# Kernel tuning notes

Hardware: AMD Instinct MI355X
Metric: run time of the kernel (lower is better)

The kernel has to match this reference:

```python
import jax, jax.numpy as jnp
import numpy as np

B, T, H, S, NH = 8, 4096, 1024, 64, 16
DH = H // NH
L = T // S  # tokens per sentence (contiguous partition)


def setup_inputs() -> dict:
    key = jax.random.key(0)
    ks = jax.random.split(key, 10)
    init = lambda k, shape: (jax.random.normal(k, shape, dtype=jnp.float32) * 0.02)
    starts = jnp.arange(S, dtype=jnp.int32) * L
    bounds = jnp.stack([starts, starts + L], axis=-1)  # [S,2]
    sentence_boundaries = jnp.broadcast_to(bounds, (B, S, 2))
    return {
        "context_hidden": jax.random.normal(ks[0], (B, T, H), dtype=jnp.float32),
        "sentence_boundaries": sentence_boundaries,
        "in_proj_w": init(ks[1], (3 * H, H)),
        "in_proj_b": jnp.zeros((3 * H,), jnp.float32),
        "out_w": init(ks[2], (H, H)),
        "out_b": jnp.zeros((H,), jnp.float32),
        "w1": init(ks[3], (H, 2 * H)),
        "b1": jnp.zeros((H,), jnp.float32),
        "w2": init(ks[4], (1, H)),
        "b2": jnp.zeros((1,), jnp.float32),
    }


def _forward(h, sentence_boundaries, in_proj_w, in_proj_b, out_w, out_b, w1, b1, w2, b2):
    starts = sentence_boundaries[:, :, 0]  # [B,S]
    ends = sentence_boundaries[:, :, 1]    # [B,S]
    t = jnp.arange(T, dtype=jnp.int32)
    # membership: token t belongs to sentence s iff start <= t < end
    member = (t[None, :, None] >= starts[:, None, :]) & (t[None, :, None] < ends[:, None, :])  # [B,T,S]
    mf = member.astype(h.dtype)
    counts = jnp.clip(mf.sum(axis=1), 1.0)  # [B,S]
    # segment mean pooling (encode_sentences)
    sent_repr = jnp.einsum('bts,bth->bsh', mf, h) / counts[..., None]  # [B,S,H]

    # multihead self-attention over sentence reprs (eval mode, no dropout)
    qkv = sent_repr @ in_proj_w.T + in_proj_b  # [B,S,3H]
    q, k, v = jnp.split(qkv, 3, axis=-1)
    q = q.reshape(B, S, NH, DH)
    k = k.reshape(B, S, NH, DH)
    v = v.reshape(B, S, NH, DH)
    scores = jnp.einsum('bqhd,bkhd->bhqk', q, k) / jnp.sqrt(jnp.asarray(DH, h.dtype))
    attn = jax.nn.softmax(scores, axis=-1)
    ctx = jnp.einsum('bhqk,bkhd->bqhd', attn, v).reshape(B, S, H)
    attended = ctx @ out_w.T + out_b  # [B,S,H]

    # gather each token's sentence repr
    sid = jnp.clip(member.astype(jnp.int32).argmax(axis=-1), 0, S - 1)  # [B,T]
    covered = member.any(axis=-1)  # [B,T]
    att_tok = jnp.take_along_axis(attended, sid[..., None], axis=1)  # [B,T,H]

    # coherence scorer MLP on concat([token, sent_repr]) without materializing concat
    hid = jax.nn.relu(h @ w1[:, :H].T + att_tok @ w1[:, H:].T + b1)  # [B,T,H]
    score = (hid @ w2.T + b2)[..., 0]  # [B,T]
    score = jnp.where(covered, score, 0.0)
    return h + score[..., None] * h


def reference(context_hidden, sentence_boundaries, in_proj_w, in_proj_b, out_w, out_b, w1, b1, w2, b2):
    return _forward(context_hidden, sentence_boundaries, in_proj_w, in_proj_b,
                    out_w, out_b, w1, b1, w2, b2)
```

## Files before the change

kernel.cpp:

```cpp
#include <hip/hip_runtime.h>
#include <stdint.h>

#define BB 8
#define TT 4096
#define HH 1024
#define SS 64
#define NHH 16
#define DHH 64

typedef __attribute__((ext_vector_type(8))) short short8;
typedef __attribute__((ext_vector_type(8))) unsigned short ushortx8;
typedef __attribute__((ext_vector_type(4))) float f32x4;
typedef unsigned short u16;

#define GLOAD16(gp, lp)                                                   \
  __builtin_amdgcn_global_load_lds(                                      \
      (const __attribute__((address_space(1))) void*)(gp),               \
      (__attribute__((address_space(3))) void*)(lp), 16, 0, 0)

__device__ __forceinline__ u16 f2bf(float f) {
  union { float f; uint32_t u; } v;
  v.f = f;
  uint32_t u = v.u;
  uint32_t r = u + 0x7fffu + ((u >> 16) & 1u);
  return (u16)(r >> 16);
}

__device__ __forceinline__ float bf2f(u16 b) {
  union { uint32_t u; float f; } v;
  v.u = ((uint32_t)b) << 16;
  return v.f;
}

__device__ __forceinline__ void stage_tile(u16* lds, const float* src, int ld, int tid) {
#pragma unroll
  for (int q = 0; q < 4; ++q) {
    int slot_id = tid + (q << 8);
    int row = slot_id >> 3;
    int sl = slot_id & 7;
    const float* p = src + (size_t)row * ld + (sl << 3);
    float4 x0 = *(const float4*)(p);
    float4 x1 = *(const float4*)(p + 4);
    ushortx8 o;
    o[0] = f2bf(x0.x); o[1] = f2bf(x0.y); o[2] = f2bf(x0.z); o[3] = f2bf(x0.w);
    o[4] = f2bf(x1.x); o[5] = f2bf(x1.y); o[6] = f2bf(x1.z); o[7] = f2bf(x1.w);
    *(ushortx8*)(&lds[(row << 6) + (((sl ^ (row & 7)) << 3))]) = o;
  }
}

__global__ __launch_bounds__(256) void conv_setup_kernel(const float* __restrict__ h,
                                                         u16* __restrict__ hbf,
                                                         const float* __restrict__ w1,
                                                         u16* __restrict__ wbf,
                                                         const float* __restrict__ ipb,
                                                         const float* __restrict__ outb,
                                                         const float* __restrict__ b1,
                                                         const int* __restrict__ bounds,
                                                         float* __restrict__ qkv,
                                                         float* __restrict__ att,
                                                         float* __restrict__ cbuf,
                                                         int* __restrict__ sid,
                                                         float* __restrict__ sent) {
  int bid = blockIdx.x;
  int tid = threadIdx.x;
  if (bid < 512) {
    int bs = bid;
    int b = bs >> 6;
    int start = bounds[bs * 2];
    int end = bounds[bs * 2 + 1];
    int lo = max(start, 0), hi = min(end, TT);
    int cnt = max(hi - lo, 0);
    float inv = 1.0f / (float)max(cnt, 1);
    const float4* h4 = (const float4*)(h) + (size_t)b * TT * 256 + tid;
    float4 a0 = {0, 0, 0, 0}, a1 = {0, 0, 0, 0}, a2 = {0, 0, 0, 0}, a3 = {0, 0, 0, 0};
    int t = lo;
    for (; t + 4 <= hi; t += 4) {
      float4 v0 = h4[(size_t)(t + 0) * 256];
      float4 v1 = h4[(size_t)(t + 1) * 256];
      float4 v2 = h4[(size_t)(t + 2) * 256];
      float4 v3 = h4[(size_t)(t + 3) * 256];
      a0.x += v0.x; a0.y += v0.y; a0.z += v0.z; a0.w += v0.w;
      a1.x += v1.x; a1.y += v1.y; a1.z += v1.z; a1.w += v1.w;
      a2.x += v2.x; a2.y += v2.y; a2.z += v2.z; a2.w += v2.w;
      a3.x += v3.x; a3.y += v3.y; a3.z += v3.z; a3.w += v3.w;
    }
    for (; t < hi; ++t) {
      float4 v0 = h4[(size_t)t * 256];
      a0.x += v0.x; a0.y += v0.y; a0.z += v0.z; a0.w += v0.w;
    }
    float4 r;
    r.x = (a0.x + a1.x + a2.x + a3.x) * inv;
    r.y = (a0.y + a1.y + a2.y + a3.y) * inv;
    r.z = (a0.z + a1.z + a2.z + a3.z) * inv;
    r.w = (a0.w + a1.w + a2.w + a3.w) * inv;
    ((float4*)sent)[(size_t)bs * 256 + tid] = r;
    return;
  }
  if (bid < 1024) {
    int sidx = (bid - 512) * 256 + tid;
    const int STR = 512 * 256;
    for (int i = sidx; i < 512 * 3072; i += STR) qkv[i] = ipb[i % 3072];
    for (int i = sidx; i < 512 * 1024; i += STR) att[i] = outb[i & 1023];
    for (int i = sidx; i < 512 * 1024; i += STR) cbuf[i] = b1[i & 1023];
    if (sidx < BB * TT) {
      int b = sidx >> 12, t = sidx & (TT - 1);
      int r = -1;
      for (int s = 0; s < SS; ++s) {
        int st = bounds[(b * SS + s) * 2], en = bounds[(b * SS + s) * 2 + 1];
        if (t >= st && t < en) { r = s; break; }
      }
      sid[sidx] = r;
    }
    return;
  }
  int tbid = bid - 1024;
  const float* src;
  int ld;
  u16* dst;
  if (tbid < 4096) { src = h;  ld = 1024; dst = hbf; }
  else             { src = w1; ld = 2048; dst = wbf; tbid -= 4096; }
  int rt = tbid >> 4, kt = tbid & 15;
  const float* s0 = src + (size_t)rt * 128 * ld + kt * 64;
  u16* d0 = dst + (size_t)tbid * 8192;
#pragma unroll
  for (int q = 0; q < 4; ++q) {
    int slot_id = tid + (q << 8);
    int row = slot_id >> 3;
    int sl = slot_id & 7;
    const float* p = s0 + (size_t)row * ld + (sl << 3);
    float4 x0 = *(const float4*)(p);
    float4 x1 = *(const float4*)(p + 4);
    ushortx8 o;
    o[0] = f2bf(x0.x); o[1] = f2bf(x0.y); o[2] = f2bf(x0.z); o[3] = f2bf(x0.w);
    o[4] = f2bf(x1.x); o[5] = f2bf(x1.y); o[6] = f2bf(x1.z); o[7] = f2bf(x1.w);
    *(ushortx8*)(&d0[(row << 6) + (((sl ^ (row & 7)) << 3))]) = o;
  }
}

__global__ __launch_bounds__(256) void gemm_bt_atomic(const float* __restrict__ A, int lda,
                                                      const float* __restrict__ Bm, int ldb,
                                                      float* __restrict__ C, int ldc,
                                                      int kper) {
  __shared__ u16 As[128 * 64];
  __shared__ u16 Bs[128 * 64];
  int tid = threadIdx.x;
  int m0 = blockIdx.x * 128, n0 = blockIdx.y * 128;
  int kbeg = blockIdx.z * kper;
  f32x4 acc[4][4] = {};

  for (int k0 = kbeg; k0 < kbeg + kper; k0 += 64) {
    __syncthreads();
    stage_tile(As, A + (size_t)m0 * lda + k0, lda, tid);
    stage_tile(Bs, Bm + (size_t)n0 * ldb + k0, ldb, tid);
    __syncthreads();
    int lane = tid & 63, wid = tid >> 6;
    int wm = wid >> 1, wn = wid & 1;
    int lr = lane & 15, lg = lane >> 4;
#pragma unroll
    for (int kk = 0; kk < 2; ++kk) {
      short8 af[4], bfr[4];
#pragma unroll
      for (int i = 0; i < 4; ++i) {
        int arow = wm * 64 + i * 16 + lr;
        int aslot = (kk * 4 + lg) ^ (arow & 7);
        af[i] = *(const short8*)(&As[(arow << 6) + (aslot << 3)]);
        int brow = wn * 64 + i * 16 + lr;
        int bslot = (kk * 4 + lg) ^ (brow & 7);
        bfr[i] = *(const short8*)(&Bs[(brow << 6) + (bslot << 3)]);
      }
#pragma unroll
      for (int i = 0; i < 4; ++i)
#pragma unroll
        for (int j = 0; j < 4; ++j)
          acc[i][j] = __builtin_amdgcn_mfma_f32_16x16x32_bf16(af[i], bfr[j], acc[i][j], 0, 0, 0);
    }
  }

  int lane = tid & 63, wid = tid >> 6;
  int wm = wid >> 1, wn = wid & 1;
  int lr = lane & 15, lg = lane >> 4;
#pragma unroll
  for (int i = 0; i < 4; ++i)
#pragma unroll
    for (int j = 0; j < 4; ++j)
#pragma unroll
      for (int r = 0; r < 4; ++r) {
        int row = m0 + wm * 64 + i * 16 + lg * 4 + r;
        int col = n0 + wn * 64 + j * 16 + lr;
        atomicAdd(&C[(size_t)row * ldc + col], acc[i][j][r]);
      }
}

#define KSW(row, col) (((row) << 6) + ((col) ^ (row)))
__global__ __launch_bounds__(256) void attn_kernel(const float* __restrict__ qkv,
                                                   float* __restrict__ ctx) {
  int bh = blockIdx.x;
  int b = bh >> 4, nh = bh & 15;
  __shared__ float q[64 * 64], k[64 * 64], v[64 * 64], s[64 * 64];
  int tid = threadIdx.x;
  const float* base = qkv + (size_t)b * SS * 3072 + nh * 64;
  for (int e = tid; e < 4096; e += 256) {
    int i = e >> 6, d = e & 63;
    q[e] = base[(size_t)i * 3072 + d];
    k[KSW(i, d)] = base[(size_t)i * 3072 + 1024 + d];
    v[e] = base[(size_t)i * 3072 + 2048 + d];
  }
  __syncthreads();
  for (int e = tid; e < 4096; e += 256) {
    int i = e >> 6, j = e & 63;
    float acc = 0.f;
#pragma unroll 8
    for (int d = 0; d < 64; ++d) acc += q[(i << 6) + d] * k[KSW(j, d)];
    s[KSW(i, j)] = acc * 0.125f;
  }
  __syncthreads();
  {
    int r = tid >> 2, sub = tid & 3;
    int j0 = sub * 16;
    float m = -1e30f;
#pragma unroll
    for (int j = 0; j < 16; ++j) m = fmaxf(m, s[KSW(r, j0 + j)]);
    m = fmaxf(m, __shfl_xor(m, 1));
    m = fmaxf(m, __shfl_xor(m, 2));
    float sum = 0.f;
#pragma unroll
    for (int j = 0; j < 16; ++j) {
      float e_ = __expf(s[KSW(r, j0 + j)] - m);
      s[KSW(r, j0 + j)] = e_;
      sum += e_;
    }
    sum += __shfl_xor(sum, 1);
    sum += __shfl_xor(sum, 2);
    float inv = 1.0f / sum;
#pragma unroll
    for (int j = 0; j < 16; ++j) s[KSW(r, j0 + j)] *= inv;
  }
  __syncthreads();
  for (int e = tid; e < 4096; e += 256) {
    int i = e >> 6, d = e & 63;
    float acc = 0.f;
#pragma unroll 8
    for (int j = 0; j < 64; ++j) acc += s[KSW(i, j)] * v[(j << 6) + d];
    ctx[((size_t)b * SS + i) * HH + nh * 64 + d] = acc;
  }
}

__global__ __launch_bounds__(512, 4) void score_partial(const u16* __restrict__ hbf,
                                                        const u16* __restrict__ wbf,
                                                        const float* __restrict__ cbuf,
                                                        const float* __restrict__ w2,
                                                        const int* __restrict__ sid_arr,
                                                        float* __restrict__ score_part) {
  __shared__ u16 As[8192];
  __shared__ u16 Bs[16384];
  __shared__ float w2_lds[256];
  __shared__ int sid_lds[128];
  __shared__ float red[128];

  int tid = threadIdx.x;
  int bid = blockIdx.x;
  int x = bid & 7;
  int g = bid >> 3;
  int mt = x * 32 + (g >> 2);
  int c = g & 3;
  int n0 = c * 256;
  size_t g0 = (size_t)mt * 128;
  int b = (int)(g0 >> 12);
  const u16* asrc = hbf + (size_t)mt * 16 * 8192;

  if (tid < 256) w2_lds[tid] = w2[n0 + tid];
  if (tid < 128) {
    sid_lds[tid] = sid_arr[g0 + tid];
    red[tid] = 0.f;
  }

  int lane = tid & 63, wid = tid >> 6;
  int wm = wid >> 2, wn = wid & 3;
  int lr = lane & 15, lg = lane >> 4;

  f32x4 acc[4][4] = {};
  for (int kt = 0; kt < 16; ++kt) {
    __syncthreads();
    const u16* at = asrc + kt * 8192;
#pragma unroll
    for (int q = 0; q < 2; ++q) {
      int off = q * 4096 + wid * 512;
      GLOAD16(at + off + lane * 8, &As[off]);
    }
#pragma unroll
    for (int q = 0; q < 4; ++q) {
      int half = q >> 1;
      int boff = (q & 1) * 4096 + wid * 512;
      const u16* bt = wbf + ((size_t)(2 * c + half) * 16 + kt) * 8192;
      GLOAD16(bt + boff + lane * 8, &Bs[half * 8192 + boff]);
    }
    __syncthreads();
#pragma unroll
    for (int kk = 0; kk < 2; ++kk) {
      short8 af[4], bfr[4];
#pragma unroll
      for (int i = 0; i < 4; ++i) {
        int arow = wm * 64 + i * 16 + lr;
        int aslot = (kk * 4 + lg) ^ (arow & 7);
        af[i] = *(const short8*)(&As[(arow << 6) + (aslot << 3)]);
      }
#pragma unroll
      for (int j = 0; j < 4; ++j) {
        int brow = wn * 64 + j * 16 + lr;
        int half = (wn * 64 + j * 16) >> 7;
        int r = brow & 127;
        int bslot = (kk * 4 + lg) ^ (r & 7);
        bfr[j] = *(const short8*)(&Bs[(half << 13) + (r << 6) + (bslot << 3)]);
      }
#pragma unroll
      for (int i = 0; i < 4; ++i)
#pragma unroll
        for (int j = 0; j < 4; ++j)
          acc[i][j] = __builtin_amdgcn_mfma_f32_16x16x32_bf16(af[i], bfr[j], acc[i][j], 0, 0, 0);
    }
  }

  float sp[4][4];
#pragma unroll
  for (int i = 0; i < 4; ++i) {
#pragma unroll
    for (int r = 0; r < 4; ++r) {
      int rowl = wm * 64 + i * 16 + lg * 4 + r;
      int s = sid_lds[rowl];
      int sc = s < 0 ? 0 : s;
      const float* crow = cbuf + ((size_t)b * SS + sc) * HH + n0;
      float accs = 0.f;
#pragma unroll
      for (int j = 0; j < 4; ++j) {
        int coll = wn * 64 + j * 16 + lr;
        float t = acc[i][j][r] + crow[coll];
        if (t > 0.f) accs += t * w2_lds[coll];
      }
      sp[i][r] = accs;
    }
  }

#pragma unroll
  for (int i = 0; i < 4; ++i)
#pragma unroll
    for (int r = 0; r < 4; ++r) {
      float v = sp[i][r];
      v += __shfl_xor(v, 1);
      v += __shfl_xor(v, 2);
      v += __shfl_xor(v, 4);
      v += __shfl_xor(v, 8);
      sp[i][r] = v;
    }
  if (lr == 0) {
#pragma unroll
    for (int i = 0; i < 4; ++i)
#pragma unroll
      for (int r = 0; r < 4; ++r)
        atomicAdd(&red[wm * 64 + i * 16 + lg * 4 + r], sp[i][r]);
  }
  __syncthreads();
  if (tid < 128) score_part[(size_t)c * (BB * TT) + g0 + tid] = red[tid];
}

__global__ __launch_bounds__(256) void scale_kernel(const u16* __restrict__ hbf,
                                                    const float* __restrict__ score_part,
                                                    const float* __restrict__ b2,
                                                    const int* __restrict__ sid_arr,
                                                    float* __restrict__ out) {
  __shared__ float fac[16];
  int tid = threadIdx.x;
  int r0 = blockIdx.x * 16;
  if (tid < 16) {
    int t = r0 + tid;
    float s = b2[0];
#pragma unroll
    for (int c = 0; c < 4; ++c) s += score_part[(size_t)c * (BB * TT) + t];
    fac[tid] = (sid_arr[t] >= 0) ? (1.0f + s) : 1.0f;
  }
  __syncthreads();
  for (int e = tid; e < 16 * 128; e += 256) {
    int row = e >> 7, grp = e & 127;
    int kt = grp >> 3, slot = grp & 7;
    int grow = r0 + row;
    int rt = grow >> 7, r = grow & 127;
    const u16* tile = hbf + ((size_t)rt * 16 + kt) * 8192;
    ushortx8 v = *(const ushortx8*)(&tile[(r << 6) + ((slot ^ (r & 7)) << 3)]);
    float f = fac[row];
    float4 o0, o1;
    o0.x = bf2f(v[0]) * f; o0.y = bf2f(v[1]) * f; o0.z = bf2f(v[2]) * f; o0.w = bf2f(v[3]) * f;
    o1.x = bf2f(v[4]) * f; o1.y = bf2f(v[5]) * f; o1.z = bf2f(v[6]) * f; o1.w = bf2f(v[7]) * f;
    float4* dst = (float4*)(out + (size_t)grow * HH + grp * 8);
    dst[0] = o0;
    dst[1] = o1;
  }
}

extern "C" void kernel_launch(void* const* d_in, const int* in_sizes, int n_in,
                              void* d_out, int out_size, void* d_ws, size_t ws_size,
                              hipStream_t stream) {
  const float* h        = (const float*)d_in[0];
  const int*   bounds   = (const int*)d_in[1];
  const float* in_proj_w = (const float*)d_in[2];
  const float* in_proj_b = (const float*)d_in[3];
  const float* out_w    = (const float*)d_in[4];
  const float* out_b    = (const float*)d_in[5];
  const float* w1       = (const float*)d_in[6];
  const float* b1       = (const float*)d_in[7];
  const float* w2       = (const float*)d_in[8];
  const float* b2       = (const float*)d_in[9];
  float* out = (float*)d_out;

  char* ws = (char*)d_ws;
  float* sent  = (float*)(ws);
  float* qkv   = (float*)(ws + (2ull << 20));
  float* ctx   = (float*)(ws + (8ull << 20));
  float* att   = (float*)(ws + (10ull << 20));
  float* cbuf  = (float*)(ws + (12ull << 20));
  int*   sid   = (int*)(ws + (14ull << 20));
  float* spart = (float*)(ws + (15ull << 20));
  u16*   hbf   = (u16*)(ws + (16ull << 20));
  u16*   wbf   = (u16*)(ws + (80ull << 20));

  conv_setup_kernel<<<512 + 512 + 4096 + 128, 256, 0, stream>>>(
      h, hbf, w1, wbf, in_proj_b, out_b, b1, bounds, qkv, att, cbuf, sid, sent);

  gemm_bt_atomic<<<dim3(4, 24, 4), 256, 0, stream>>>(sent, HH, in_proj_w, HH, qkv, 3 * HH, 256);
  attn_kernel<<<BB * NHH, 256, 0, stream>>>(qkv, ctx);
  gemm_bt_atomic<<<dim3(4, 8, 4), 256, 0, stream>>>(ctx, HH, out_w, HH, att, HH, 256);
  gemm_bt_atomic<<<dim3(4, 8, 4), 256, 0, stream>>>(att, HH, w1 + HH, 2 * HH, cbuf, HH, 256);

  score_partial<<<1024, 512, 0, stream>>>(hbf, wbf, cbuf, w2, sid, spart);
  scale_kernel<<<2048, 256, 0, stream>>>(hbf, spart, b2, sid, out);
}
```

Baseline: 268.6 us.

## Fold out-projection into W1 second half to drop one sentence-level GEMM

Precomputes M = W1[:,H:] @ out_w in bf16 and a folded bias b1 + W1[:,H:] @ out_b inside the setup kernel. The ctx-to-cbuf path then needs one GEMM instead of two chained ones, and the bias is added in the score epilogue. This removes a kernel launch and its atomic accumulation pass. The cost is an extra 1024x1024x1024 weight GEMM on every call, run in 64 blocks of the setup kernel with a scattered transposed LDS store, plus one more bf16 rounding step on the fused weights.

```diff
diff --git a/kernel.cpp b/kernel.cpp
--- a/kernel.cpp
+++ b/kernel.cpp
@@ -48,23 +48,104 @@
   }
 }
 
+__device__ __forceinline__ void stage_tile_bf(u16* lds, const u16* src, int ld, int tid) {
+#pragma unroll
+  for (int q = 0; q < 4; ++q) {
+    int slot_id = tid + (q << 8);
+    int row = slot_id >> 3;
+    int sl = slot_id & 7;
+    ushortx8 v = *(const ushortx8*)(src + (size_t)row * ld + (sl << 3));
+    *(ushortx8*)(&lds[(row << 6) + (((sl ^ (row & 7)) << 3))]) = v;
+  }
+}
+
 __global__ __launch_bounds__(256) void conv_setup_kernel(const float* __restrict__ h,
                                                          u16* __restrict__ hbf,
                                                          const float* __restrict__ w1,
                                                          u16* __restrict__ wbf,
+                                                         const float* __restrict__ outw,
+                                                         const float* __restrict__ outb,
                                                          const float* __restrict__ ipb,
-                                                         const float* __restrict__ outb,
                                                          const float* __restrict__ b1,
                                                          const int* __restrict__ bounds,
                                                          float* __restrict__ qkv,
-                                                         float* __restrict__ att,
                                                          float* __restrict__ cbuf,
                                                          int* __restrict__ sid,
-                                                         float* __restrict__ sent) {
+                                                         float* __restrict__ sent,
+                                                         u16* __restrict__ Mbf,
+                                                         float* __restrict__ biasp) {
+  __shared__ u16 As[8192];
+  __shared__ u16 Bs[8192];
   int bid = blockIdx.x;
   int tid = threadIdx.x;
-  if (bid < 512) {
-    int bs = bid;
+  if (bid < 64) {
+    int m0 = (bid >> 3) * 128, n0 = (bid & 7) * 128;
+    f32x4 acc[4][4] = {};
+    int lane = tid & 63, wid = tid >> 6;
+    int wm = wid >> 1, wn = wid & 1;
+    int lr = lane & 15, lg = lane >> 4;
+    for (int r0 = 0; r0 < 1024; r0 += 64) {
+      __syncthreads();
+      stage_tile(As, w1 + 1024 + (size_t)m0 * 2048 + r0, 2048, tid);
+      for (int u = tid; u < 1024; u += 256) {
+        int rr = u >> 4, cg = (u & 15) << 3;
+        const float* p = outw + (size_t)(r0 + rr) * 1024 + n0 + cg;
+        float4 x0 = *(const float4*)(p);
+        float4 x1 = *(const float4*)(p + 4);
+        float vals[8] = {x0.x, x0.y, x0.z, x0.w, x1.x, x1.y, x1.z, x1.w};
+        int rhi = rr >> 3, rlo = rr & 7;
+#pragma unroll
+        for (int m = 0; m < 8; ++m) {
+          int cc = cg + m;
+          Bs[(cc << 6) + ((rhi ^ (cc & 7)) << 3) + rlo] = f2bf(vals[m]);
+        }
+      }
+      __syncthreads();
+#pragma unroll
+      for (int kk = 0; kk < 2; ++kk) {
+        short8 af[4], bfr[4];
+#pragma unroll
+        for (int i = 0; i < 4; ++i) {
+          int arow = wm * 64 + i * 16 + lr;
+          int aslot = (kk * 4 + lg) ^ (arow & 7);
+          af[i] = *(const short8*)(&As[(arow << 6) + (aslot << 3)]);
+          int brow = wn * 64 + i * 16 + lr;
+          int bslot = (kk * 4 + lg) ^ (brow & 7);
+          bfr[i] = *(const short8*)(&Bs[(brow << 6) + (bslot << 3)]);
+        }
+#pragma unroll
+        for (int i = 0; i < 4; ++i)
+#pragma unroll
+          for (int j = 0; j < 4; ++j)
+            acc[i][j] = __builtin_amdgcn_mfma_f32_16x16x32_bf16(af[i], bfr[j], acc[i][j], 0, 0, 0);
+      }
+    }
+#pragma unroll
+    for (int i = 0; i < 4; ++i)
+#pragma unroll
+      for (int j = 0; j < 4; ++j)
+#pragma unroll
+        for (int r = 0; r < 4; ++r) {
+          int row = m0 + wm * 64 + i * 16 + lg * 4 + r;
+          int col = n0 + wn * 64 + j * 16 + lr;
+          Mbf[(size_t)row * 1024 + col] = f2bf(acc[i][j][r]);
+        }
+    return;
+  }
+  if (bid < 68) {
+    int row = (bid - 64) * 256 + tid;
+    const float* wrow = w1 + (size_t)row * 2048 + 1024;
+    float s = b1[row];
+    for (int k = 0; k < 1024; k += 4) {
+      float4 wv = *(const float4*)(wrow + k);
+      float4 ov = *(const float4*)(outb + k);
+      s += wv.x * ov.x + wv.y * ov.y + wv.z * ov.z + wv.w * ov.w;
+    }
+    biasp[row] = s;
+    return;
+  }
+  if (bid < 580) {
+    int bs = bid - 68;
     int b = bs >> 6;
     int start = bounds[bs * 2];
     int end = bounds[bs * 2 + 1];
@@ -96,12 +177,15 @@
     ((float4*)sent)[(size_t)bs * 256 + tid] = r;
     return;
   }
-  if (bid < 1024) {
-    int sidx = (bid - 512) * 256 + tid;
+  if (bid < 1092) {
+    int sidx = (bid - 580) * 256 + tid;
     const int STR = 512 * 256;
-    for (int i = sidx; i < 512 * 3072; i += STR) qkv[i] = ipb[i % 3072];
-    for (int i = sidx; i < 512 * 1024; i += STR) att[i] = outb[i & 1023];
-    for (int i = sidx; i < 512 * 1024; i += STR) cbuf[i] = b1[i & 1023];
+    float4* qkv4 = (float4*)qkv;
+    const float4* ipb4 = (const float4*)ipb;
+    for (int i = sidx; i < 512 * 768; i += STR) qkv4[i] = ipb4[i % 768];
+    float4 z = {0.f, 0.f, 0.f, 0.f};
+    float4* cbuf4 = (float4*)cbuf;
+    for (int i = sidx; i < 512 * 256; i += STR) cbuf4[i] = z;
     if (sidx < BB * TT) {
       int b = sidx >> 12, t = sidx & (TT - 1);
       int r = -1;
@@ -113,7 +197,7 @@
     }
     return;
   }
-  int tbid = bid - 1024;
+  int tbid = bid - 1092;
   const float* src;
   int ld;
   u16* dst;
@@ -152,6 +236,60 @@
     __syncthreads();
     stage_tile(As, A + (size_t)m0 * lda + k0, lda, tid);
     stage_tile(Bs, Bm + (size_t)n0 * ldb + k0, ldb, tid);
+    __syncthreads();
+    int lane = tid & 63, wid = tid >> 6;
+    int wm = wid >> 1, wn = wid & 1;
+    int lr = lane & 15, lg = lane >> 4;
+#pragma unroll
+    for (int kk = 0; kk < 2; ++kk) {
+      short8 af[4], bfr[4];
+#pragma unroll
+      for (int i = 0; i < 4; ++i) {
+        int arow = wm * 64 + i * 16 + lr;
+        int aslot = (kk * 4 + lg) ^ (arow & 7);
+        af[i] = *(const short8*)(&As[(arow << 6) + (aslot << 3)]);
+        int brow = wn * 64 + i * 16 + lr;
+        int bslot = (kk * 4 + lg) ^ (brow & 7);
+        bfr[i] = *(const short8*)(&Bs[(brow << 6) + (bslot << 3)]);
+      }
+#pragma unroll
+      for (int i = 0; i < 4; ++i)
+#pragma unroll
+        for (int j = 0; j < 4; ++j)
+          acc[i][j] = __builtin_amdgcn_mfma_f32_16x16x32_bf16(af[i], bfr[j], acc[i][j], 0, 0, 0);
+    }
+  }
+
+  int lane = tid & 63, wid = tid >> 6;
+  int wm = wid >> 1, wn = wid & 1;
+  int lr = lane & 15, lg = lane >> 4;
+#pragma unroll
+  for (int i = 0; i < 4; ++i)
+#pragma unroll
+    for (int j = 0; j < 4; ++j)
+#pragma unroll
+      for (int r = 0; r < 4; ++r) {
+        int row = m0 + wm * 64 + i * 16 + lg * 4 + r;
+        int col = n0 + wn * 64 + j * 16 + lr;
+        atomicAdd(&C[(size_t)row * ldc + col], acc[i][j][r]);
+      }
+}
+
+__global__ __launch_bounds__(256) void gemm_btbf_atomic(const float* __restrict__ A, int lda,
+                                                        const u16* __restrict__ Bm, int ldb,
+                                                        float* __restrict__ C, int ldc,
+                                                        int kper) {
+  __shared__ u16 As[128 * 64];
+  __shared__ u16 Bs[128 * 64];
+  int tid = threadIdx.x;
+  int m0 = blockIdx.x * 128, n0 = blockIdx.y * 128;
+  int kbeg = blockIdx.z * kper;
+  f32x4 acc[4][4] = {};
+
+  for (int k0 = kbeg; k0 < kbeg + kper; k0 += 64) {
+    __syncthreads();
+    stage_tile(As, A + (size_t)m0 * lda + k0, lda, tid);
+    stage_tile_bf(Bs, Bm + (size_t)n0 * ldb + k0, ldb, tid);
     __syncthreads();
     int lane = tid & 63, wid = tid >> 6;
     int wm = wid >> 1, wn = wid & 1;
@@ -249,11 +387,13 @@
                                                         const u16* __restrict__ wbf,
                                                         const float* __restrict__ cbuf,
                                                         const float* __restrict__ w2,
+                                                        const float* __restrict__ biasp,
                                                         const int* __restrict__ sid_arr,
                                                         float* __restrict__ score_part) {
   __shared__ u16 As[8192];
   __shared__ u16 Bs[16384];
   __shared__ float w2_lds[256];
+  __shared__ float bp_lds[256];
   __shared__ int sid_lds[128];
   __shared__ float red[128];
 
@@ -268,7 +408,10 @@
   int b = (int)(g0 >> 12);
   const u16* asrc = hbf + (size_t)mt * 16 * 8192;
 
-  if (tid < 256) w2_lds[tid] = w2[n0 + tid];
+  if (tid < 256) {
+    w2_lds[tid] = w2[n0 + tid];
+    bp_lds[tid] = biasp[n0 + tid];
+  }
   if (tid < 128) {
     sid_lds[tid] = sid_arr[g0 + tid];
     red[tid] = 0.f;
@@ -333,7 +476,7 @@
 #pragma unroll
       for (int j = 0; j < 4; ++j) {
         int coll = wn * 64 + j * 16 + lr;
-        float t = acc[i][j][r] + crow[coll];
+        float t = acc[i][j][r] + crow[coll] + bp_lds[coll];
         if (t > 0.f) accs += t * w2_lds[coll];
       }
       sp[i][r] = accs;
@@ -414,21 +557,22 @@
   float* sent  = (float*)(ws);
   float* qkv   = (float*)(ws + (2ull << 20));
   float* ctx   = (float*)(ws + (8ull << 20));
-  float* att   = (float*)(ws + (10ull << 20));
+  u16*   Mbf   = (u16*)(ws + (10ull << 20));
   float* cbuf  = (float*)(ws + (12ull << 20));
   int*   sid   = (int*)(ws + (14ull << 20));
+  float* biasp = (float*)(ws + (14ull << 20) + (256 << 10));
   float* spart = (float*)(ws + (15ull << 20));
   u16*   hbf   = (u16*)(ws + (16ull << 20));
   u16*   wbf   = (u16*)(ws + (80ull << 20));
 
-  conv_setup_kernel<<<512 + 512 + 4096 + 128, 256, 0, stream>>>(
-      h, hbf, w1, wbf, in_proj_b, out_b, b1, bounds, qkv, att, cbuf, sid, sent);
+  conv_setup_kernel<<<64 + 4 + 512 + 512 + 4224, 256, 0, stream>>>(
+      h, hbf, w1, wbf, out_w, out_b, in_proj_b, b1, bounds,
+      qkv, cbuf, sid, sent, Mbf, biasp);
 
   gemm_bt_atomic<<<dim3(4, 24, 4), 256, 0, stream>>>(sent, HH, in_proj_w, HH, qkv, 3 * HH, 256);
   attn_kernel<<<BB * NHH, 256, 0, stream>>>(qkv, ctx);
-  gemm_bt_atomic<<<dim3(4, 8, 4), 256, 0, stream>>>(ctx, HH, out_w, HH, att, HH, 256);
-  gemm_bt_atomic<<<dim3(4, 8, 4), 256, 0, stream>>>(att, HH, w1 + HH, 2 * HH, cbuf, HH, 256);
-
-  score_partial<<<1024, 512, 0, stream>>>(hbf, wbf, cbuf, w2, sid, spart);
+  gemm_btbf_atomic<<<dim3(4, 8, 4), 256, 0, stream>>>(ctx, HH, Mbf, HH, cbuf, HH, 256);
+
+  score_partial<<<1024, 512, 0, stream>>>(hbf, wbf, cbuf, w2, biasp, sid, spart);
   scale_kernel<<<2048, 256, 0, stream>>>(hbf, spart, b2, sid, out);
 }
```

New measurement: 283.2 us. +5.5%, slower.
